# Kernel optimization log

Measured on AMD Instinct MI355X. Metric: run time of the kernel, lower is better.

The kernel has to match this reference:

```python
import jax, jax.numpy as jnp
import numpy as np

MASK_VALUE = -1000000.0  # matches torch source's value=-1000000.0


def setup_inputs() -> dict:
    key = jax.random.key(0)
    kq, kk, kv, kl = jax.random.split(key, 4)
    B, S, D = 64, 1024, 64
    q = jax.random.normal(kq, (B, S, D), dtype=jnp.float32)
    k = jax.random.normal(kk, (B, S, D), dtype=jnp.float32)
    v = jax.random.normal(kv, (B, S, D), dtype=jnp.float32)
    valid_lens = jax.random.randint(kl, (B,), 0, S, dtype=jnp.int32)
    return {"q": q, "k": k, "v": v, "valid_lens": valid_lens}


def reference(q, k, v, valid_lens):
    # scores: [B, Sq, Sk]
    d = q.shape[-1]
    scores = jnp.einsum("bqd,bkd->bqk", q, k) / jnp.sqrt(jnp.float32(d))
    # 1-D valid_lens broadcast over the query dim (torch repeat_interleave branch)
    Sk = k.shape[1]
    mask = jnp.arange(Sk, dtype=jnp.int32)[None, None, :] < valid_lens[:, None, None]
    scores = jnp.where(mask, scores, MASK_VALUE)
    attn = jax.nn.softmax(scores, axis=-1)
    # dropout p=0.0 -> identity (eval-mode reference)
    return jnp.einsum("bqk,bkd->bqd", attn, v)
```

## Files before the change

### kernel.cpp

```cpp
#include <hip/hip_runtime.h>
#include <math.h>


#define BATCH 64
#define SEQ   1024
#define DIM   64
#define BQ    64
#define BC    32
#define NKT   (SEQ / BC)
#define KSTR  72
#define VSTR  40
#define PSTR  40
#define NITEMS (BATCH * (SEQ / BQ))
#define GRID  768
#define QSCALE 0.18033688011112442f
#define MASKED -1.0e6f

typedef __attribute__((ext_vector_type(8))) short bf16x8;
typedef __attribute__((ext_vector_type(4))) float f32x4;

__device__ __forceinline__ uint pack2_trunc(float lo, float hi) {
    return __builtin_amdgcn_perm(__float_as_uint(hi), __float_as_uint(lo), 0x07060302);
}
__device__ __forceinline__ ushort f2bf_rne(float x) {
    uint u = __float_as_uint(x);
    return (ushort)((u + 0x7fffu + ((u >> 16) & 1u)) >> 16);
}

__global__ __launch_bounds__(256, 3) void attn_mfma_flash4(
    const float* __restrict__ q, const float* __restrict__ k,
    const float* __restrict__ v, const int* __restrict__ valid_lens,
    float* __restrict__ out, unsigned* __restrict__ cnt)
{
    __shared__ ushort Ks[BC * KSTR];
    __shared__ ushort Vt[DIM * VSTR];
    __shared__ ushort Ps[BQ * PSTR];
    __shared__ int next_item;

    const int t    = threadIdx.x;
    const int wave = t >> 6;
    const int wl   = t & 63;
    const int QD   = wl >> 4;
    const int li   = wl & 15;

    int item = blockIdx.x;
    while (item < NITEMS) {
        const int b  = item & 63;
        const int q0 = (item >> 6) * BQ;
        const int vl = valid_lens[b];
        const size_t boff = (size_t)b * SEQ * DIM;

        bf16x8 qb[2];
        {
            const float* qrow = q + boff + (size_t)(q0 + wave * 16 + li) * DIM + QD * 8;
            #pragma unroll
            for (int kc = 0; kc < 2; kc++) {
                float4 a = *(const float4*)(qrow + kc * 32);
                float4 c = *(const float4*)(qrow + kc * 32 + 4);
                union { bf16x8 v; ushort u[8]; } tmp;
                tmp.u[0] = f2bf_rne(a.x * QSCALE);
                tmp.u[1] = f2bf_rne(a.y * QSCALE);
                tmp.u[2] = f2bf_rne(a.z * QSCALE);
                tmp.u[3] = f2bf_rne(a.w * QSCALE);
                tmp.u[4] = f2bf_rne(c.x * QSCALE);
                tmp.u[5] = f2bf_rne(c.y * QSCALE);
                tmp.u[6] = f2bf_rne(c.z * QSCALE);
                tmp.u[7] = f2bf_rne(c.w * QSCALE);
                qb[kc] = tmp.v;
            }
        }

        const int it_max = (vl == 0) ? NKT : ((vl + BC - 1) / BC);

        float4 kf[2];
        float  vf[8];

        auto load_tile = [&](int it) {
            const float4* kg = (const float4*)(k + boff + (size_t)it * BC * DIM);
            kf[0] = kg[t];
            kf[1] = kg[t + 256];
            const float* vgf = v + boff + (size_t)it * BC * DIM;
            #pragma unroll
            for (int j = 0; j < 8; j++)
                vf[j] = vgf[(size_t)(wave * 8 + j) * DIM + wl];
        };
        auto stage = [&]() {
            #pragma unroll
            for (int i = 0; i < 2; i++) {
                int idx = t + 256 * i;
                int row = idx >> 4, c4 = idx & 15;
                uint2 w;
                w.x = pack2_trunc(kf[i].x, kf[i].y);
                w.y = pack2_trunc(kf[i].z, kf[i].w);
                *(uint2*)&Ks[row * KSTR + c4 * 4] = w;
            }
            uint4 wv;
            wv.x = pack2_trunc(vf[0], vf[1]);
            wv.y = pack2_trunc(vf[2], vf[3]);
            wv.z = pack2_trunc(vf[4], vf[5]);
            wv.w = pack2_trunc(vf[6], vf[7]);
            *(uint4*)&Vt[wl * VSTR + wave * 8] = wv;
        };

        float m_run = -INFINITY, l_run = 0.f;
        f32x4 acc[4];
        #pragma unroll
        for (int dt = 0; dt < 4; dt++) acc[dt] = (f32x4){0.f, 0.f, 0.f, 0.f};

        load_tile(0);
        stage();
        if (it_max > 1) load_tile(1);
        __syncthreads();

        for (int it = 0; it < it_max; it++) {
            bf16x8 ka[2][2], vb[4];
            #pragma unroll
            for (int kt = 0; kt < 2; kt++) {
                ka[kt][0] = *(const bf16x8*)&Ks[(kt * 16 + li) * KSTR + QD * 8];
                ka[kt][1] = *(const bf16x8*)&Ks[(kt * 16 + li) * KSTR + 32 + QD * 8];
            }
            #pragma unroll
            for (int dt = 0; dt < 4; dt++)
                vb[dt] = *(const bf16x8*)&Vt[(dt * 16 + li) * VSTR + QD * 8];
            __syncthreads();

            if (it + 1 < it_max) stage();
            if (it + 2 < it_max) load_tile(it + 2);

            f32x4 sc[2];
            #pragma unroll
            for (int kt = 0; kt < 2; kt++) {
                f32x4 c = (f32x4){0.f, 0.f, 0.f, 0.f};
                c = __builtin_amdgcn_mfma_f32_16x16x32_bf16(ka[kt][0], qb[0], c, 0, 0, 0);
                c = __builtin_amdgcn_mfma_f32_16x16x32_bf16(ka[kt][1], qb[1], c, 0, 0, 0);
                sc[kt] = c;
            }

            const int kbase = it * BC;
            if (kbase + BC > vl) {
                #pragma unroll
                for (int kt = 0; kt < 2; kt++)
                    #pragma unroll
                    for (int r = 0; r < 4; r++) {
                        int key = kbase + kt * 16 + QD * 4 + r;
                        if (key >= vl) sc[kt][r] = MASKED;
                    }
            }

            float mt = -INFINITY;
            #pragma unroll
            for (int kt = 0; kt < 2; kt++)
                #pragma unroll
                for (int r = 0; r < 4; r++) mt = fmaxf(mt, sc[kt][r]);
            mt = fmaxf(mt, __shfl_xor(mt, 16, 64));
            mt = fmaxf(mt, __shfl_xor(mt, 32, 64));
            float mn = fmaxf(m_run, mt);
            float alpha = exp2f(m_run - mn);
            m_run = mn;

            float ls = 0.f;
            #pragma unroll
            for (int kt = 0; kt < 2; kt++) {
                float p0 = exp2f(sc[kt][0] - mn);
                float p1 = exp2f(sc[kt][1] - mn);
                float p2 = exp2f(sc[kt][2] - mn);
                float p3 = exp2f(sc[kt][3] - mn);
                ls += (p0 + p1) + (p2 + p3);
                uint2 w;
                w.x = pack2_trunc(p0, p1);
                w.y = pack2_trunc(p2, p3);
                *(uint2*)&Ps[(wave * 16 + li) * PSTR + kt * 16 + QD * 4] = w;
            }
            ls += __shfl_xor(ls, 16, 64);
            ls += __shfl_xor(ls, 32, 64);
            l_run = l_run * alpha + ls;

            float a0 = __shfl(alpha, QD * 4 + 0, 64);
            float a1 = __shfl(alpha, QD * 4 + 1, 64);
            float a2 = __shfl(alpha, QD * 4 + 2, 64);
            float a3 = __shfl(alpha, QD * 4 + 3, 64);
            #pragma unroll
            for (int dt = 0; dt < 4; dt++) {
                acc[dt][0] *= a0; acc[dt][1] *= a1;
                acc[dt][2] *= a2; acc[dt][3] *= a3;
            }

            bf16x8 pa = *(const bf16x8*)&Ps[(wave * 16 + li) * PSTR + QD * 8];
            #pragma unroll
            for (int dt = 0; dt < 4; dt++)
                acc[dt] = __builtin_amdgcn_mfma_f32_16x16x32_bf16(pa, vb[dt], acc[dt], 0, 0, 0);

            __syncthreads();
        }

        float invl = 1.0f / l_run;
        float i0 = __shfl(invl, QD * 4 + 0, 64);
        float i1 = __shfl(invl, QD * 4 + 1, 64);
        float i2 = __shfl(invl, QD * 4 + 2, 64);
        float i3 = __shfl(invl, QD * 4 + 3, 64);
        float* ob = out + boff + (size_t)q0 * DIM;
        const int rbase = wave * 16 + QD * 4;
        #pragma unroll
        for (int dt = 0; dt < 4; dt++) {
            int col = dt * 16 + li;
            ob[(size_t)(rbase + 0) * DIM + col] = acc[dt][0] * i0;
            ob[(size_t)(rbase + 1) * DIM + col] = acc[dt][1] * i1;
            ob[(size_t)(rbase + 2) * DIM + col] = acc[dt][2] * i2;
            ob[(size_t)(rbase + 3) * DIM + col] = acc[dt][3] * i3;
        }

        if (t == 0) next_item = GRID + (int)atomicAdd(cnt, 1u);
        __syncthreads();
        item = next_item;
    }
}

extern "C" void kernel_launch(void* const* d_in, const int* in_sizes, int n_in,
                              void* d_out, int out_size, void* d_ws, size_t ws_size,
                              hipStream_t stream) {
    const float* q = (const float*)d_in[0];
    const float* k = (const float*)d_in[1];
    const float* v = (const float*)d_in[2];
    const int* valid_lens = (const int*)d_in[3];
    float* out = (float*)d_out;
    unsigned* cnt = (unsigned*)d_ws;

    hipMemsetAsync(cnt, 0, sizeof(unsigned), stream);
    attn_mfma_flash4<<<dim3(GRID), dim3(256), 0, stream>>>(q, k, v, valid_lens, out, cnt);
}
```

Measured before the change: 135.4 us.

## Restructure attention into independent per-wave flash tiles without block barriers

Each wave now owns 32 query rows as two 16-row bands and stages its own K tile in private LDS, so the block-wide __syncthreads per key tile go away. V is read straight from global into registers in MFMA operand layout instead of through transposed LDS. The persistent atomic work queue and its memset are replaced by a static grid of 2-wave blocks. In exchange, each wave loads K and V redundantly, so global/L2 traffic per query goes up, and load balancing across uneven valid lengths is left to the hardware scheduler.

```diff
diff --git a/kernel.cpp b/kernel.cpp
--- a/kernel.cpp
+++ b/kernel.cpp
@@ -5,14 +5,11 @@
 #define BATCH 64
 #define SEQ   1024
 #define DIM   64
-#define BQ    64
+#define WQ    32
 #define BC    32
 #define NKT   (SEQ / BC)
 #define KSTR  72
-#define VSTR  40
 #define PSTR  40
-#define NITEMS (BATCH * (SEQ / BQ))
-#define GRID  768
 #define QSCALE 0.18033688011112442f
 #define MASKED -1.0e6f
 
@@ -27,153 +24,156 @@
     return (ushort)((u + 0x7fffu + ((u >> 16) & 1u)) >> 16);
 }
 
-__global__ __launch_bounds__(256, 3) void attn_mfma_flash4(
+__global__ __launch_bounds__(128, 2) void attn_waveflash(
     const float* __restrict__ q, const float* __restrict__ k,
     const float* __restrict__ v, const int* __restrict__ valid_lens,
-    float* __restrict__ out, unsigned* __restrict__ cnt)
+    float* __restrict__ out)
 {
-    __shared__ ushort Ks[BC * KSTR];
-    __shared__ ushort Vt[DIM * VSTR];
-    __shared__ ushort Ps[BQ * PSTR];
-    __shared__ int next_item;
+    __shared__ ushort Ks[2][BC * KSTR];
+    __shared__ ushort Ps[2][WQ * PSTR];
 
     const int t    = threadIdx.x;
-    const int wave = t >> 6;
+    const int wv   = t >> 6;
     const int wl   = t & 63;
     const int QD   = wl >> 4;
     const int li   = wl & 15;
 
-    int item = blockIdx.x;
-    while (item < NITEMS) {
-        const int b  = item & 63;
-        const int q0 = (item >> 6) * BQ;
-        const int vl = valid_lens[b];
-        const size_t boff = (size_t)b * SEQ * DIM;
-
-        bf16x8 qb[2];
-        {
-            const float* qrow = q + boff + (size_t)(q0 + wave * 16 + li) * DIM + QD * 8;
-            #pragma unroll
-            for (int kc = 0; kc < 2; kc++) {
-                float4 a = *(const float4*)(qrow + kc * 32);
-                float4 c = *(const float4*)(qrow + kc * 32 + 4);
-                union { bf16x8 v; ushort u[8]; } tmp;
-                tmp.u[0] = f2bf_rne(a.x * QSCALE);
-                tmp.u[1] = f2bf_rne(a.y * QSCALE);
-                tmp.u[2] = f2bf_rne(a.z * QSCALE);
-                tmp.u[3] = f2bf_rne(a.w * QSCALE);
-                tmp.u[4] = f2bf_rne(c.x * QSCALE);
-                tmp.u[5] = f2bf_rne(c.y * QSCALE);
-                tmp.u[6] = f2bf_rne(c.z * QSCALE);
-                tmp.u[7] = f2bf_rne(c.w * QSCALE);
-                qb[kc] = tmp.v;
-            }
-        }
-
-        const int it_max = (vl == 0) ? NKT : ((vl + BC - 1) / BC);
-
-        float4 kf[2];
-        float  vf[8];
-
-        auto load_tile = [&](int it) {
-            const float4* kg = (const float4*)(k + boff + (size_t)it * BC * DIM);
-            kf[0] = kg[t];
-            kf[1] = kg[t + 256];
-            const float* vgf = v + boff + (size_t)it * BC * DIM;
+    const int gw = blockIdx.x * 2 + wv;
+    const int b  = gw >> 5;
+    const int q0 = (gw & 31) * WQ;
+    const int vl = valid_lens[b];
+    const size_t boff = (size_t)b * SEQ * DIM;
+
+    ushort* ks = Ks[wv];
+    ushort* ps = Ps[wv];
+
+    bf16x8 qb[2][2];
+    #pragma unroll
+    for (int band = 0; band < 2; band++) {
+        const float* qrow = q + boff + (size_t)(q0 + band * 16 + li) * DIM + QD * 8;
+        #pragma unroll
+        for (int h = 0; h < 2; h++) {
+            float4 a = *(const float4*)(qrow + h * 32);
+            float4 c = *(const float4*)(qrow + h * 32 + 4);
+            union { bf16x8 v; ushort u[8]; } tmp;
+            tmp.u[0] = f2bf_rne(a.x * QSCALE);
+            tmp.u[1] = f2bf_rne(a.y * QSCALE);
+            tmp.u[2] = f2bf_rne(a.z * QSCALE);
+            tmp.u[3] = f2bf_rne(a.w * QSCALE);
+            tmp.u[4] = f2bf_rne(c.x * QSCALE);
+            tmp.u[5] = f2bf_rne(c.y * QSCALE);
+            tmp.u[6] = f2bf_rne(c.z * QSCALE);
+            tmp.u[7] = f2bf_rne(c.w * QSCALE);
+            qb[band][h] = tmp.v;
+        }
+    }
+
+    const int it_max = (vl == 0) ? NKT : ((vl + BC - 1) / BC);
+
+    const int krow = wl >> 1;
+    const int kcol = (wl & 1) * 32;
+    float4 kpf[8];
+    auto load_k = [&](int it) {
+        const float4* kg = (const float4*)(k + boff + (size_t)it * BC * DIM);
+        #pragma unroll
+        for (int i = 0; i < 8; i++)
+            kpf[i] = kg[krow * 16 + (wl & 1) * 8 + i];
+    };
+    auto stage_k = [&]() {
+        #pragma unroll
+        for (int j = 0; j < 4; j++) {
+            uint4 w;
+            w.x = pack2_trunc(kpf[2 * j].x, kpf[2 * j].y);
+            w.y = pack2_trunc(kpf[2 * j].z, kpf[2 * j].w);
+            w.z = pack2_trunc(kpf[2 * j + 1].x, kpf[2 * j + 1].y);
+            w.w = pack2_trunc(kpf[2 * j + 1].z, kpf[2 * j + 1].w);
+            *(uint4*)&ks[krow * KSTR + kcol + j * 8] = w;
+        }
+    };
+
+    float m_run[2] = {-INFINITY, -INFINITY};
+    float l_run[2] = {0.f, 0.f};
+    f32x4 acc[2][4];
+    #pragma unroll
+    for (int band = 0; band < 2; band++)
+        #pragma unroll
+        for (int dt = 0; dt < 4; dt++) acc[band][dt] = (f32x4){0.f, 0.f, 0.f, 0.f};
+
+    load_k(0);
+    stage_k();
+    if (it_max > 1) load_k(1);
+
+    for (int it = 0; it < it_max; it++) {
+        bf16x8 ka[2][2];
+        #pragma unroll
+        for (int kt = 0; kt < 2; kt++)
+            #pragma unroll
+            for (int h = 0; h < 2; h++)
+                ka[kt][h] = *(const bf16x8*)&ks[(kt * 16 + li) * KSTR + h * 32 + QD * 8];
+
+        if (it + 1 < it_max) stage_k();
+        if (it + 2 < it_max) load_k(it + 2);
+
+        const float* vg = v + boff + (size_t)it * BC * DIM;
+        float vf[4][8];
+        #pragma unroll
+        for (int dt = 0; dt < 4; dt++)
             #pragma unroll
             for (int j = 0; j < 8; j++)
-                vf[j] = vgf[(size_t)(wave * 8 + j) * DIM + wl];
-        };
-        auto stage = [&]() {
-            #pragma unroll
-            for (int i = 0; i < 2; i++) {
-                int idx = t + 256 * i;
-                int row = idx >> 4, c4 = idx & 15;
-                uint2 w;
-                w.x = pack2_trunc(kf[i].x, kf[i].y);
-                w.y = pack2_trunc(kf[i].z, kf[i].w);
-                *(uint2*)&Ks[row * KSTR + c4 * 4] = w;
-            }
-            uint4 wv;
-            wv.x = pack2_trunc(vf[0], vf[1]);
-            wv.y = pack2_trunc(vf[2], vf[3]);
-            wv.z = pack2_trunc(vf[4], vf[5]);
-            wv.w = pack2_trunc(vf[6], vf[7]);
-            *(uint4*)&Vt[wl * VSTR + wave * 8] = wv;
-        };
-
-        float m_run = -INFINITY, l_run = 0.f;
-        f32x4 acc[4];
-        #pragma unroll
-        for (int dt = 0; dt < 4; dt++) acc[dt] = (f32x4){0.f, 0.f, 0.f, 0.f};
-
-        load_tile(0);
-        stage();
-        if (it_max > 1) load_tile(1);
-        __syncthreads();
-
-        for (int it = 0; it < it_max; it++) {
-            bf16x8 ka[2][2], vb[4];
+                vf[dt][j] = vg[(size_t)(QD * 8 + j) * DIM + dt * 16 + li];
+
+        f32x4 sc[2][2];
+        #pragma unroll
+        for (int kt = 0; kt < 2; kt++)
+            #pragma unroll
+            for (int band = 0; band < 2; band++) {
+                f32x4 c = (f32x4){0.f, 0.f, 0.f, 0.f};
+                c = __builtin_amdgcn_mfma_f32_16x16x32_bf16(ka[kt][0], qb[band][0], c, 0, 0, 0);
+                c = __builtin_amdgcn_mfma_f32_16x16x32_bf16(ka[kt][1], qb[band][1], c, 0, 0, 0);
+                sc[kt][band] = c;
+            }
+
+        const int kbase = it * BC;
+        if (kbase + BC > vl) {
             #pragma unroll
             for (int kt = 0; kt < 2; kt++) {
-                ka[kt][0] = *(const bf16x8*)&Ks[(kt * 16 + li) * KSTR + QD * 8];
-                ka[kt][1] = *(const bf16x8*)&Ks[(kt * 16 + li) * KSTR + 32 + QD * 8];
-            }
-            #pragma unroll
-            for (int dt = 0; dt < 4; dt++)
-                vb[dt] = *(const bf16x8*)&Vt[(dt * 16 + li) * VSTR + QD * 8];
-            __syncthreads();
-
-            if (it + 1 < it_max) stage();
-            if (it + 2 < it_max) load_tile(it + 2);
-
-            f32x4 sc[2];
-            #pragma unroll
-            for (int kt = 0; kt < 2; kt++) {
-                f32x4 c = (f32x4){0.f, 0.f, 0.f, 0.f};
-                c = __builtin_amdgcn_mfma_f32_16x16x32_bf16(ka[kt][0], qb[0], c, 0, 0, 0);
-                c = __builtin_amdgcn_mfma_f32_16x16x32_bf16(ka[kt][1], qb[1], c, 0, 0, 0);
-                sc[kt] = c;
-            }
-
-            const int kbase = it * BC;
-            if (kbase + BC > vl) {
                 #pragma unroll
-                for (int kt = 0; kt < 2; kt++)
-                    #pragma unroll
-                    for (int r = 0; r < 4; r++) {
-                        int key = kbase + kt * 16 + QD * 4 + r;
-                        if (key >= vl) sc[kt][r] = MASKED;
-                    }
-            }
-
+                for (int r = 0; r < 4; r++) {
+                    int key = kbase + kt * 16 + QD * 4 + r;
+                    if (key >= vl) { sc[kt][0][r] = MASKED; sc[kt][1][r] = MASKED; }
+                }
+            }
+        }
+
+        #pragma unroll
+        for (int band = 0; band < 2; band++) {
             float mt = -INFINITY;
             #pragma unroll
             for (int kt = 0; kt < 2; kt++)
                 #pragma unroll
-                for (int r = 0; r < 4; r++) mt = fmaxf(mt, sc[kt][r]);
+                for (int r = 0; r < 4; r++) mt = fmaxf(mt, sc[kt][band][r]);
             mt = fmaxf(mt, __shfl_xor(mt, 16, 64));
             mt = fmaxf(mt, __shfl_xor(mt, 32, 64));
-            float mn = fmaxf(m_run, mt);
-            float alpha = exp2f(m_run - mn);
-            m_run = mn;
+            float mn = fmaxf(m_run[band], mt);
+            float alpha = exp2f(m_run[band] - mn);
+            m_run[band] = mn;
 
             float ls = 0.f;
             #pragma unroll
             for (int kt = 0; kt < 2; kt++) {
-                float p0 = exp2f(sc[kt][0] - mn);
-                float p1 = exp2f(sc[kt][1] - mn);
-                float p2 = exp2f(sc[kt][2] - mn);
-                float p3 = exp2f(sc[kt][3] - mn);
+                float p0 = exp2f(sc[kt][band][0] - mn);
+                float p1 = exp2f(sc[kt][band][1] - mn);
+                float p2 = exp2f(sc[kt][band][2] - mn);
+                float p3 = exp2f(sc[kt][band][3] - mn);
                 ls += (p0 + p1) + (p2 + p3);
                 uint2 w;
                 w.x = pack2_trunc(p0, p1);
                 w.y = pack2_trunc(p2, p3);
-                *(uint2*)&Ps[(wave * 16 + li) * PSTR + kt * 16 + QD * 4] = w;
+                *(uint2*)&ps[(band * 16 + li) * PSTR + kt * 16 + QD * 4] = w;
             }
             ls += __shfl_xor(ls, 16, 64);
             ls += __shfl_xor(ls, 32, 64);
-            l_run = l_run * alpha + ls;
+            l_run[band] = l_run[band] * alpha + ls;
 
             float a0 = __shfl(alpha, QD * 4 + 0, 64);
             float a1 = __shfl(alpha, QD * 4 + 1, 64);
@@ -181,37 +181,45 @@
             float a3 = __shfl(alpha, QD * 4 + 3, 64);
             #pragma unroll
             for (int dt = 0; dt < 4; dt++) {
-                acc[dt][0] *= a0; acc[dt][1] *= a1;
-                acc[dt][2] *= a2; acc[dt][3] *= a3;
-            }
-
-            bf16x8 pa = *(const bf16x8*)&Ps[(wave * 16 + li) * PSTR + QD * 8];
-            #pragma unroll
-            for (int dt = 0; dt < 4; dt++)
-                acc[dt] = __builtin_amdgcn_mfma_f32_16x16x32_bf16(pa, vb[dt], acc[dt], 0, 0, 0);
-
-            __syncthreads();
-        }
-
-        float invl = 1.0f / l_run;
+                acc[band][dt][0] *= a0; acc[band][dt][1] *= a1;
+                acc[band][dt][2] *= a2; acc[band][dt][3] *= a3;
+            }
+        }
+
+        bf16x8 pa[2];
+        #pragma unroll
+        for (int band = 0; band < 2; band++)
+            pa[band] = *(const bf16x8*)&ps[(band * 16 + li) * PSTR + QD * 8];
+        #pragma unroll
+        for (int dt = 0; dt < 4; dt++) {
+            union { bf16x8 v; uint u[4]; } vb;
+            vb.u[0] = pack2_trunc(vf[dt][0], vf[dt][1]);
+            vb.u[1] = pack2_trunc(vf[dt][2], vf[dt][3]);
+            vb.u[2] = pack2_trunc(vf[dt][4], vf[dt][5]);
+            vb.u[3] = pack2_trunc(vf[dt][6], vf[dt][7]);
+            #pragma unroll
+            for (int band = 0; band < 2; band++)
+                acc[band][dt] = __builtin_amdgcn_mfma_f32_16x16x32_bf16(pa[band], vb.v, acc[band][dt], 0, 0, 0);
+        }
+    }
+
+    float* ob = out + boff + (size_t)q0 * DIM;
+    #pragma unroll
+    for (int band = 0; band < 2; band++) {
+        float invl = 1.0f / l_run[band];
         float i0 = __shfl(invl, QD * 4 + 0, 64);
         float i1 = __shfl(invl, QD * 4 + 1, 64);
         float i2 = __shfl(invl, QD * 4 + 2, 64);
         float i3 = __shfl(invl, QD * 4 + 3, 64);
-        float* ob = out + boff + (size_t)q0 * DIM;
-        const int rbase = wave * 16 + QD * 4;
+        const int rbase = band * 16 + QD * 4;
         #pragma unroll
         for (int dt = 0; dt < 4; dt++) {
             int col = dt * 16 + li;
-            ob[(size_t)(rbase + 0) * DIM + col] = acc[dt][0] * i0;
-            ob[(size_t)(rbase + 1) * DIM + col] = acc[dt][1] * i1;
-            ob[(size_t)(rbase + 2) * DIM + col] = acc[dt][2] * i2;
-            ob[(size_t)(rbase + 3) * DIM + col] = acc[dt][3] * i3;
-        }
-
-        if (t == 0) next_item = GRID + (int)atomicAdd(cnt, 1u);
-        __syncthreads();
-        item = next_item;
+            ob[(size_t)(rbase + 0) * DIM + col] = acc[band][dt][0] * i0;
+            ob[(size_t)(rbase + 1) * DIM + col] = acc[band][dt][1] * i1;
+            ob[(size_t)(rbase + 2) * DIM + col] = acc[band][dt][2] * i2;
+            ob[(size_t)(rbase + 3) * DIM + col] = acc[band][dt][3] * i3;
+        }
     }
 }
 
@@ -223,8 +231,7 @@
     const float* v = (const float*)d_in[2];
     const int* valid_lens = (const int*)d_in[3];
     float* out = (float*)d_out;
-    unsigned* cnt = (unsigned*)d_ws;
-
-    hipMemsetAsync(cnt, 0, sizeof(unsigned), stream);
-    attn_mfma_flash4<<<dim3(GRID), dim3(256), 0, stream>>>(q, k, v, valid_lens, out, cnt);
-}
+
+    attn_waveflash<<<dim3(BATCH * (SEQ / WQ) / 2), dim3(128), 0, stream>>>(
+        q, k, v, valid_lens, out);
+}
```

Result: slower. 157.6 us (+16.4%).

## Double-buffer K/V LDS tiles and replace persistent atomic scheduler with full grid

Applied to the files above, without the earlier changes.

Drops the persistent-kernel work queue (atomic counter plus memset) and launches one block per (batch, query-tile) item. K and V LDS tiles are now double-buffered, so each iteration needs one barrier instead of two and next-tile staging happens after the PV MFMA. The register prefetch depth falls from two tiles to one, and launch bounds go from 3 to 2 blocks per CU. This loses the dynamic load balancing over variable valid_lens and may hide less global-memory latency.

```diff
diff --git a/kernel.cpp b/kernel.cpp
--- a/kernel.cpp
+++ b/kernel.cpp
@@ -11,8 +11,6 @@
 #define KSTR  72
 #define VSTR  40
 #define PSTR  40
-#define NITEMS (BATCH * (SEQ / BQ))
-#define GRID  768
 #define QSCALE 0.18033688011112442f
 #define MASKED -1.0e6f
 
@@ -27,191 +25,181 @@
     return (ushort)((u + 0x7fffu + ((u >> 16) & 1u)) >> 16);
 }
 
-__global__ __launch_bounds__(256, 3) void attn_mfma_flash4(
+__global__ __launch_bounds__(256, 2) void attn_mfma_flash6(
     const float* __restrict__ q, const float* __restrict__ k,
     const float* __restrict__ v, const int* __restrict__ valid_lens,
-    float* __restrict__ out, unsigned* __restrict__ cnt)
+    float* __restrict__ out)
 {
-    __shared__ ushort Ks[BC * KSTR];
-    __shared__ ushort Vt[DIM * VSTR];
+    __shared__ ushort Ks[2][BC * KSTR];
+    __shared__ ushort Vt[2][DIM * VSTR];
     __shared__ ushort Ps[BQ * PSTR];
-    __shared__ int next_item;
 
     const int t    = threadIdx.x;
     const int wave = t >> 6;
     const int wl   = t & 63;
     const int QD   = wl >> 4;
     const int li   = wl & 15;
-
-    int item = blockIdx.x;
-    while (item < NITEMS) {
-        const int b  = item & 63;
-        const int q0 = (item >> 6) * BQ;
-        const int vl = valid_lens[b];
-        const size_t boff = (size_t)b * SEQ * DIM;
-
-        bf16x8 qb[2];
-        {
-            const float* qrow = q + boff + (size_t)(q0 + wave * 16 + li) * DIM + QD * 8;
-            #pragma unroll
-            for (int kc = 0; kc < 2; kc++) {
-                float4 a = *(const float4*)(qrow + kc * 32);
-                float4 c = *(const float4*)(qrow + kc * 32 + 4);
-                union { bf16x8 v; ushort u[8]; } tmp;
-                tmp.u[0] = f2bf_rne(a.x * QSCALE);
-                tmp.u[1] = f2bf_rne(a.y * QSCALE);
-                tmp.u[2] = f2bf_rne(a.z * QSCALE);
-                tmp.u[3] = f2bf_rne(a.w * QSCALE);
-                tmp.u[4] = f2bf_rne(c.x * QSCALE);
-                tmp.u[5] = f2bf_rne(c.y * QSCALE);
-                tmp.u[6] = f2bf_rne(c.z * QSCALE);
-                tmp.u[7] = f2bf_rne(c.w * QSCALE);
-                qb[kc] = tmp.v;
-            }
-        }
-
-        const int it_max = (vl == 0) ? NKT : ((vl + BC - 1) / BC);
-
-        float4 kf[2];
-        float  vf[8];
-
-        auto load_tile = [&](int it) {
-            const float4* kg = (const float4*)(k + boff + (size_t)it * BC * DIM);
-            kf[0] = kg[t];
-            kf[1] = kg[t + 256];
-            const float* vgf = v + boff + (size_t)it * BC * DIM;
-            #pragma unroll
-            for (int j = 0; j < 8; j++)
-                vf[j] = vgf[(size_t)(wave * 8 + j) * DIM + wl];
-        };
-        auto stage = [&]() {
-            #pragma unroll
-            for (int i = 0; i < 2; i++) {
-                int idx = t + 256 * i;
-                int row = idx >> 4, c4 = idx & 15;
-                uint2 w;
-                w.x = pack2_trunc(kf[i].x, kf[i].y);
-                w.y = pack2_trunc(kf[i].z, kf[i].w);
-                *(uint2*)&Ks[row * KSTR + c4 * 4] = w;
-            }
-            uint4 wv;
-            wv.x = pack2_trunc(vf[0], vf[1]);
-            wv.y = pack2_trunc(vf[2], vf[3]);
-            wv.z = pack2_trunc(vf[4], vf[5]);
-            wv.w = pack2_trunc(vf[6], vf[7]);
-            *(uint4*)&Vt[wl * VSTR + wave * 8] = wv;
-        };
-
-        float m_run = -INFINITY, l_run = 0.f;
-        f32x4 acc[4];
-        #pragma unroll
-        for (int dt = 0; dt < 4; dt++) acc[dt] = (f32x4){0.f, 0.f, 0.f, 0.f};
-
-        load_tile(0);
-        stage();
-        if (it_max > 1) load_tile(1);
+    const int b    = blockIdx.x & 63;
+    const int q0   = (blockIdx.x >> 6) * BQ;
+    const int vl   = valid_lens[b];
+    const size_t boff = (size_t)b * SEQ * DIM;
+
+    bf16x8 qb[2];
+    {
+        const float* qrow = q + boff + (size_t)(q0 + wave * 16 + li) * DIM + QD * 8;
+        #pragma unroll
+        for (int h = 0; h < 2; h++) {
+            float4 a = *(const float4*)(qrow + h * 32);
+            float4 c = *(const float4*)(qrow + h * 32 + 4);
+            union { bf16x8 v; ushort u[8]; } tmp;
+            tmp.u[0] = f2bf_rne(a.x * QSCALE);
+            tmp.u[1] = f2bf_rne(a.y * QSCALE);
+            tmp.u[2] = f2bf_rne(a.z * QSCALE);
+            tmp.u[3] = f2bf_rne(a.w * QSCALE);
+            tmp.u[4] = f2bf_rne(c.x * QSCALE);
+            tmp.u[5] = f2bf_rne(c.y * QSCALE);
+            tmp.u[6] = f2bf_rne(c.z * QSCALE);
+            tmp.u[7] = f2bf_rne(c.w * QSCALE);
+            qb[h] = tmp.v;
+        }
+    }
+
+    const int it_max = (vl == 0) ? NKT : ((vl + BC - 1) / BC);
+
+    float4 kf[2];
+    float  vf[8];
+
+    auto load_tile = [&](int it) {
+        const float4* kg = (const float4*)(k + boff + (size_t)it * BC * DIM);
+        kf[0] = kg[t];
+        kf[1] = kg[t + 256];
+        const float* vgf = v + boff + (size_t)it * BC * DIM;
+        #pragma unroll
+        for (int j = 0; j < 8; j++)
+            vf[j] = vgf[(size_t)(wave * 8 + j) * DIM + wl];
+    };
+    auto stage = [&](int pb) {
+        #pragma unroll
+        for (int i = 0; i < 2; i++) {
+            int idx = t + 256 * i;
+            int row = idx >> 4, c4 = idx & 15;
+            uint2 w;
+            w.x = pack2_trunc(kf[i].x, kf[i].y);
+            w.y = pack2_trunc(kf[i].z, kf[i].w);
+            *(uint2*)&Ks[pb][row * KSTR + c4 * 4] = w;
+        }
+        uint4 wv;
+        wv.x = pack2_trunc(vf[0], vf[1]);
+        wv.y = pack2_trunc(vf[2], vf[3]);
+        wv.z = pack2_trunc(vf[4], vf[5]);
+        wv.w = pack2_trunc(vf[6], vf[7]);
+        *(uint4*)&Vt[pb][wl * VSTR + wave * 8] = wv;
+    };
+
+    float m_run = -INFINITY, l_run = 0.f;
+    f32x4 acc[4];
+    #pragma unroll
+    for (int dt = 0; dt < 4; dt++) acc[dt] = (f32x4){0.f, 0.f, 0.f, 0.f};
+
+    load_tile(0);
+    stage(0);
+
+    for (int it = 0; it < it_max; it++) {
+        const int p = it & 1;
         __syncthreads();
 
-        for (int it = 0; it < it_max; it++) {
-            bf16x8 ka[2][2], vb[4];
-            #pragma unroll
-            for (int kt = 0; kt < 2; kt++) {
-                ka[kt][0] = *(const bf16x8*)&Ks[(kt * 16 + li) * KSTR + QD * 8];
-                ka[kt][1] = *(const bf16x8*)&Ks[(kt * 16 + li) * KSTR + 32 + QD * 8];
-            }
-            #pragma unroll
-            for (int dt = 0; dt < 4; dt++)
-                vb[dt] = *(const bf16x8*)&Vt[(dt * 16 + li) * VSTR + QD * 8];
-            __syncthreads();
-
-            if (it + 1 < it_max) stage();
-            if (it + 2 < it_max) load_tile(it + 2);
-
-            f32x4 sc[2];
-            #pragma unroll
-            for (int kt = 0; kt < 2; kt++) {
-                f32x4 c = (f32x4){0.f, 0.f, 0.f, 0.f};
-                c = __builtin_amdgcn_mfma_f32_16x16x32_bf16(ka[kt][0], qb[0], c, 0, 0, 0);
-                c = __builtin_amdgcn_mfma_f32_16x16x32_bf16(ka[kt][1], qb[1], c, 0, 0, 0);
-                sc[kt] = c;
-            }
-
-            const int kbase = it * BC;
-            if (kbase + BC > vl) {
-                #pragma unroll
-                for (int kt = 0; kt < 2; kt++)
-                    #pragma unroll
-                    for (int r = 0; r < 4; r++) {
-                        int key = kbase + kt * 16 + QD * 4 + r;
-                        if (key >= vl) sc[kt][r] = MASKED;
-                    }
-            }
-
-            float mt = -INFINITY;
+        bf16x8 ka[2][2], vb[4];
+        #pragma unroll
+        for (int kt = 0; kt < 2; kt++) {
+            ka[kt][0] = *(const bf16x8*)&Ks[p][(kt * 16 + li) * KSTR + QD * 8];
+            ka[kt][1] = *(const bf16x8*)&Ks[p][(kt * 16 + li) * KSTR + 32 + QD * 8];
+        }
+        #pragma unroll
+        for (int dt = 0; dt < 4; dt++)
+            vb[dt] = *(const bf16x8*)&Vt[p][(dt * 16 + li) * VSTR + QD * 8];
+
+        if (it + 1 < it_max) load_tile(it + 1);
+
+        f32x4 sc[2];
+        #pragma unroll
+        for (int kt = 0; kt < 2; kt++) {
+            f32x4 c = (f32x4){0.f, 0.f, 0.f, 0.f};
+            c = __builtin_amdgcn_mfma_f32_16x16x32_bf16(ka[kt][0], qb[0], c, 0, 0, 0);
+            c = __builtin_amdgcn_mfma_f32_16x16x32_bf16(ka[kt][1], qb[1], c, 0, 0, 0);
+            sc[kt] = c;
+        }
+
+        const int kbase = it * BC;
+        if (kbase + BC > vl) {
             #pragma unroll
             for (int kt = 0; kt < 2; kt++)
                 #pragma unroll
-                for (int r = 0; r < 4; r++) mt = fmaxf(mt, sc[kt][r]);
-            mt = fmaxf(mt, __shfl_xor(mt, 16, 64));
-            mt = fmaxf(mt, __shfl_xor(mt, 32, 64));
-            float mn = fmaxf(m_run, mt);
-            float alpha = exp2f(m_run - mn);
-            m_run = mn;
-
-            float ls = 0.f;
+                for (int r = 0; r < 4; r++) {
+                    int key = kbase + kt * 16 + QD * 4 + r;
+                    if (key >= vl) sc[kt][r] = MASKED;
+                }
+        }
+
+        float mt = -INFINITY;
+        #pragma unroll
+        for (int kt = 0; kt < 2; kt++)
             #pragma unroll
-            for (int kt = 0; kt < 2; kt++) {
-                float p0 = exp2f(sc[kt][0] - mn);
-                float p1 = exp2f(sc[kt][1] - mn);
-                float p2 = exp2f(sc[kt][2] - mn);
-                float p3 = exp2f(sc[kt][3] - mn);
-                ls += (p0 + p1) + (p2 + p3);
-                uint2 w;
-                w.x = pack2_trunc(p0, p1);
-                w.y = pack2_trunc(p2, p3);
-                *(uint2*)&Ps[(wave * 16 + li) * PSTR + kt * 16 + QD * 4] = w;
-            }
-            ls += __shfl_xor(ls, 16, 64);
-            ls += __shfl_xor(ls, 32, 64);
-            l_run = l_run * alpha + ls;
-
-            float a0 = __shfl(alpha, QD * 4 + 0, 64);
-            float a1 = __shfl(alpha, QD * 4 + 1, 64);
-            float a2 = __shfl(alpha, QD * 4 + 2, 64);
-            float a3 = __shfl(alpha, QD * 4 + 3, 64);
-            #pragma unroll
-            for (int dt = 0; dt < 4; dt++) {
-                acc[dt][0] *= a0; acc[dt][1] *= a1;
-                acc[dt][2] *= a2; acc[dt][3] *= a3;
-            }
-
-            bf16x8 pa = *(const bf16x8*)&Ps[(wave * 16 + li) * PSTR + QD * 8];
-            #pragma unroll
-            for (int dt = 0; dt < 4; dt++)
-                acc[dt] = __builtin_amdgcn_mfma_f32_16x16x32_bf16(pa, vb[dt], acc[dt], 0, 0, 0);
-
-            __syncthreads();
-        }
-
-        float invl = 1.0f / l_run;
-        float i0 = __shfl(invl, QD * 4 + 0, 64);
-        float i1 = __shfl(invl, QD * 4 + 1, 64);
-        float i2 = __shfl(invl, QD * 4 + 2, 64);
-        float i3 = __shfl(invl, QD * 4 + 3, 64);
-        float* ob = out + boff + (size_t)q0 * DIM;
-        const int rbase = wave * 16 + QD * 4;
+            for (int r = 0; r < 4; r++) mt = fmaxf(mt, sc[kt][r]);
+        mt = fmaxf(mt, __shfl_xor(mt, 16, 64));
+        mt = fmaxf(mt, __shfl_xor(mt, 32, 64));
+        float mn = fmaxf(m_run, mt);
+        float alpha = exp2f(m_run - mn);
+        m_run = mn;
+
+        float ls = 0.f;
+        #pragma unroll
+        for (int kt = 0; kt < 2; kt++) {
+            float p0 = exp2f(sc[kt][0] - mn);
+            float p1 = exp2f(sc[kt][1] - mn);
+            float p2 = exp2f(sc[kt][2] - mn);
+            float p3 = exp2f(sc[kt][3] - mn);
+            ls += (p0 + p1) + (p2 + p3);
+            uint2 w;
+            w.x = pack2_trunc(p0, p1);
+            w.y = pack2_trunc(p2, p3);
+            *(uint2*)&Ps[(wave * 16 + li) * PSTR + kt * 16 + QD * 4] = w;
+        }
+        ls += __shfl_xor(ls, 16, 64);
+        ls += __shfl_xor(ls, 32, 64);
+        l_run = l_run * alpha + ls;
+
+        float a0 = __shfl(alpha, QD * 4 + 0, 64);
+        float a1 = __shfl(alpha, QD * 4 + 1, 64);
+        float a2 = __shfl(alpha, QD * 4 + 2, 64);
+        float a3 = __shfl(alpha, QD * 4 + 3, 64);
         #pragma unroll
         for (int dt = 0; dt < 4; dt++) {
-            int col = dt * 16 + li;
-            ob[(size_t)(rbase + 0) * DIM + col] = acc[dt][0] * i0;
-            ob[(size_t)(rbase + 1) * DIM + col] = acc[dt][1] * i1;
-            ob[(size_t)(rbase + 2) * DIM + col] = acc[dt][2] * i2;
-            ob[(size_t)(rbase + 3) * DIM + col] = acc[dt][3] * i3;
-        }
-
-        if (t == 0) next_item = GRID + (int)atomicAdd(cnt, 1u);
-        __syncthreads();
-        item = next_item;
+            acc[dt][0] *= a0; acc[dt][1] *= a1;
+            acc[dt][2] *= a2; acc[dt][3] *= a3;
+        }
+
+        bf16x8 pa = *(const bf16x8*)&Ps[(wave * 16 + li) * PSTR + QD * 8];
+        #pragma unroll
+        for (int dt = 0; dt < 4; dt++)
+            acc[dt] = __builtin_amdgcn_mfma_f32_16x16x32_bf16(pa, vb[dt], acc[dt], 0, 0, 0);
+
+        if (it + 1 < it_max) stage(p ^ 1);
+    }
+
+    float invl = 1.0f / l_run;
+    float i0 = __shfl(invl, QD * 4 + 0, 64);
+    float i1 = __shfl(invl, QD * 4 + 1, 64);
+    float i2 = __shfl(invl, QD * 4 + 2, 64);
+    float i3 = __shfl(invl, QD * 4 + 3, 64);
+    float* ob = out + boff + (size_t)q0 * DIM;
+    const int rbase = wave * 16 + QD * 4;
+    #pragma unroll
+    for (int dt = 0; dt < 4; dt++) {
+        int col = dt * 16 + li;
+        ob[(size_t)(rbase + 0) * DIM + col] = acc[dt][0] * i0;
+        ob[(size_t)(rbase + 1) * DIM + col] = acc[dt][1] * i1;
+        ob[(size_t)(rbase + 2) * DIM + col] = acc[dt][2] * i2;
+        ob[(size_t)(rbase + 3) * DIM + col] = acc[dt][3] * i3;
     }
 }
 
@@ -223,8 +211,7 @@
     const float* v = (const float*)d_in[2];
     const int* valid_lens = (const int*)d_in[3];
     float* out = (float*)d_out;
-    unsigned* cnt = (unsigned*)d_ws;
-
-    hipMemsetAsync(cnt, 0, sizeof(unsigned), stream);
-    attn_mfma_flash4<<<dim3(GRID), dim3(256), 0, stream>>>(q, k, v, valid_lens, out, cnt);
-}
+
+    attn_mfma_flash6<<<dim3(BATCH * (SEQ / BQ)), dim3(256), 0, stream>>>(
+        q, k, v, valid_lens, out);
+}
```

Result: faster. 132.6 us (-2.1%).
